# Kernel tuning notes

Measured on AMD Instinct MI355X. Metric: run time of the kernel, lower is better.

The kernel has to match this reference:

```python
import jax, jax.numpy as jnp
import numpy as np

B, S, D = 4, 2048, 768
H, K = 12, 64

def setup_inputs() -> dict:
    key = jax.random.key(0)
    k1, k2, k3, k4 = jax.random.split(key, 4)
    x = jax.random.normal(k1, (B, S, D), dtype=jnp.float32)
    Wq = jax.random.normal(k2, (H, D, K), dtype=jnp.float32) * 0.02
    Wk = jax.random.normal(k3, (H, D, K), dtype=jnp.float32) * 0.02
    Wv = jax.random.normal(k4, (H, D, K), dtype=jnp.float32) * 0.02
    return {"x": x, "Wq": Wq, "Wk": Wk, "Wv": Wv}

def reference(x, Wq, Wk, Wv):
    # per-head projections (batched over heads): [B,H,S,K]
    q = jnp.einsum('bsd,hdk->bhsk', x, Wq)
    k = jnp.einsum('bsd,hdk->bhsk', x, Wk)
    v = jnp.einsum('bsd,hdk->bhsk', x, Wv)
    scale = 1.0 / jnp.sqrt(jnp.float32(q.shape[-1]))
    scores = jnp.einsum('bhsk,bhtk->bhst', q, k) * scale  # [B,H,S,S]
    causal = jnp.tril(jnp.ones((x.shape[1], x.shape[1]), dtype=bool))
    scores = jnp.where(causal, scores, jnp.float32(-jnp.inf))
    wei = jax.nn.softmax(scores, axis=-1)
    out = jnp.einsum('bhst,bhtk->bhsk', wei, v)  # [B,H,S,K]
    # concat heads on last dim, matching torch.cat([head(x)...], dim=-1)
    b, h, s, kk = out.shape
    return out.transpose(0, 2, 1, 3).reshape(b, s, h * kk)
```

## Files before the change

### kernel.cpp

```cpp
#include <hip/hip_runtime.h>
#include <math.h>

#define BB 4
#define SS 2048
#define DD 768
#define HH 12
#define KK 64

#define NPROJ 3
#define HK    (HH * KK)
#define NCOLS (NPROJ * HK)
#define MROWS (BB * SS)
#define PER   (BB * HH * SS * KK)

typedef __attribute__((ext_vector_type(8))) short bf16x8;
typedef __attribute__((ext_vector_type(4))) short bf16x4;
typedef __attribute__((ext_vector_type(4))) float f32x4;
typedef __attribute__((ext_vector_type(16))) float f32x16;

static __device__ __forceinline__ short f2bf(float f) {
  union { float f; unsigned u; } v;
  v.f = f;
  unsigned r = (v.u + 0x7fff + ((v.u >> 16) & 1)) >> 16;
  return (short)r;
}

static __device__ __forceinline__ unsigned cvtpk(float lo, float hi) {
  unsigned r;
  asm("v_cvt_pk_bf16_f32 %0, %1, %2" : "=v"(r) : "v"(lo), "v"(hi));
  return r;
}

static __device__ __forceinline__ float fexp2(float x) {
#if __has_builtin(__builtin_amdgcn_exp2f)
  return __builtin_amdgcn_exp2f(x);
#else
  return exp2f(x);
#endif
}

__global__ __launch_bounds__(256) void conv_x(const float* __restrict__ x,
                                              short* __restrict__ xbf) {
  int i = (blockIdx.x * 256 + threadIdx.x) * 8;
  float4 v0 = *(const float4*)(x + i);
  float4 v1 = *(const float4*)(x + i + 4);
  bf16x8 o = {f2bf(v0.x), f2bf(v0.y), f2bf(v0.z), f2bf(v0.w),
              f2bf(v1.x), f2bf(v1.y), f2bf(v1.z), f2bf(v1.w)};
  *(bf16x8*)(xbf + i) = o;
}

__global__ __launch_bounds__(256) void conv_w(const float* __restrict__ Wq,
                                              const float* __restrict__ Wk,
                                              const float* __restrict__ Wv,
                                              short* __restrict__ wbf) {
  int o = blockIdx.x * 256 + threadIdx.x;
  int n = o / DD, d = o % DD;
  int proj = n / HK;
  int hk = n % HK;
  int h = hk >> 6, k = hk & 63;
  const float* W = proj == 0 ? Wq : (proj == 1 ? Wk : Wv);
  float v = W[(size_t)h * DD * KK + (size_t)d * KK + k];
  if (proj == 0) v *= 0.125f * 1.44269504088896340736f;
  wbf[o] = f2bf(v);
}

__global__ __launch_bounds__(256) void qkv_gemm(const short* __restrict__ xbf,
                                                const short* __restrict__ wbf,
                                                short* __restrict__ qkv) {
  __shared__ short smem[4 * 128 * 64];
  int bid = blockIdx.x;
  int i = bid >> 3;
  int bm = (bid & 7) * 8 + (i & 7);
  int bn = i >> 3;
  int m0 = bm * 128, n0 = bn * 128;
  int tid = threadIdx.x, lane = tid & 63, wid = tid >> 6;
  int li = lane & 15, lg = lane >> 4;
  int wm = wid >> 1, wn = wid & 1;

  f32x4 acc[4][4];
  #pragma unroll
  for (int mi = 0; mi < 4; ++mi)
    #pragma unroll
    for (int ni = 0; ni < 4; ++ni)
      acc[mi][ni] = (f32x4){0.f, 0.f, 0.f, 0.f};

  int rowoff = lane >> 3;
  int kpsw = ((lane & 7) ^ rowoff) * 8;

  #define GSTAGE(bf_, kt_)                                                     \
    {                                                                          \
      short* As_ = smem + (bf_) * 16384;                                       \
      short* Bs_ = As_ + 8192;                                                 \
      _Pragma("unroll")                                                        \
      for (int j = 0; j < 4; ++j) {                                            \
        int eb = wid * 2048 + j * 512;                                         \
        int row = (eb >> 6) + rowoff;                                          \
        __builtin_amdgcn_global_load_lds(                                      \
            (const __attribute__((address_space(1))) void*)(                   \
                xbf + (size_t)(m0 + row) * DD + (kt_) * 64 + kpsw),            \
            (__attribute__((address_space(3))) void*)(As_ + eb), 16, 0, 0);    \
        __builtin_amdgcn_global_load_lds(                                      \
            (const __attribute__((address_space(1))) void*)(                   \
                wbf + (size_t)(n0 + row) * DD + (kt_) * 64 + kpsw),            \
            (__attribute__((address_space(3))) void*)(Bs_ + eb), 16, 0, 0);    \
      }                                                                        \
    }

  GSTAGE(0, 0);

  for (int kt = 0; kt < DD / 64; ++kt) {
    int cur = kt & 1;
    if (kt + 1 < DD / 64) {
      GSTAGE(cur ^ 1, kt + 1);
      asm volatile("s_waitcnt vmcnt(8)" ::: "memory");
    } else {
      asm volatile("s_waitcnt vmcnt(0)" ::: "memory");
    }
    __builtin_amdgcn_s_barrier();

    const short* As = smem + cur * 16384;
    const short* Bs = As + 8192;
    #pragma unroll
    for (int kk = 0; kk < 2; ++kk) {
      bf16x8 af[4], bfr[4];
      #pragma unroll
      for (int mi = 0; mi < 4; ++mi)
        af[mi] = *(const bf16x8*)(As + (wm * 64 + mi * 16 + li) * 64 +
                                  (((kk * 4 + lg) ^ (li & 7)) << 3));
      #pragma unroll
      for (int ni = 0; ni < 4; ++ni)
        bfr[ni] = *(const bf16x8*)(Bs + (wn * 64 + ni * 16 + li) * 64 +
                                   (((kk * 4 + lg) ^ (li & 7)) << 3));
      #pragma unroll
      for (int mi = 0; mi < 4; ++mi)
        #pragma unroll
        for (int ni = 0; ni < 4; ++ni)
          acc[mi][ni] = __builtin_amdgcn_mfma_f32_16x16x32_bf16(
              af[mi], bfr[ni], acc[mi][ni], 0, 0, 0);
    }
    __builtin_amdgcn_s_barrier();
  }
  #undef GSTAGE

  int proj = n0 / HK;
  int hk0 = n0 % HK;
  int h0 = hk0 >> 6;

  if (proj == 2) {
    #pragma unroll
    for (int ni = 0; ni < 4; ++ni) {
      int ncol = n0 + wn * 64 + ni * 16 + li;
      int hk = ncol % HK;
      int h = hk >> 6, k = hk & 63;
      #pragma unroll
      for (int mi = 0; mi < 4; ++mi) {
        int mrow0 = m0 + wm * 64 + mi * 16 + lg * 4;
        int b = mrow0 >> 11, s = mrow0 & 2047;
        bf16x4 o = {f2bf(acc[mi][ni][0]), f2bf(acc[mi][ni][1]),
                    f2bf(acc[mi][ni][2]), f2bf(acc[mi][ni][3])};
        *(bf16x4*)(qkv + 2 * (size_t)PER +
                   ((size_t)(b * HH + h) * KK + k) * SS + s) = o;
      }
    }
  } else {
    short* Cs = smem;
    __syncthreads();
    #pragma unroll
    for (int ni = 0; ni < 4; ++ni) {
      int nl = wn * 64 + ni * 16 + li;
      int slot = nl >> 3, nlo = nl & 7;
      #pragma unroll
      for (int mi = 0; mi < 4; ++mi) {
        int ml0 = wm * 64 + mi * 16 + lg * 4;
        #pragma unroll
        for (int r = 0; r < 4; ++r) {
          int ml = ml0 + r;
          Cs[ml * 128 + ((slot ^ (ml & 7)) << 3) + nlo] =
              f2bf(acc[mi][ni][r]);
        }
      }
    }
    __syncthreads();
    int sl = tid & 7;
    #pragma unroll
    for (int p = 0; p < 8; ++p) {
      int line = p * 32 + (tid >> 3);
      int hh = line >> 7, mrow = line & 127;
      bf16x8 v = *(const bf16x8*)&Cs[mrow * 128 +
                                     (((hh * 8 + sl) ^ (mrow & 7)) << 3)];
      int gm = m0 + mrow;
      int b = gm >> 11, s = gm & 2047;
      *(bf16x8*)(qkv + (size_t)proj * PER +
                 ((size_t)(b * HH + h0 + hh) * SS + s) * KK + sl * 8) = v;
    }
  }
}

static __device__ __forceinline__ void attn_step_lds(
    const short* Kt, const short* Vv, const bf16x8* qf, bool diag, int h2,
    int lq, int hi, float& lsum, f32x16& acc0, f32x16& acc1) {
  int x7 = lq & 7;
  bf16x8 kf[4];
  {
    int kbase = (h2 * 32 + lq) * 64;
    #pragma unroll
    for (int c = 0; c < 4; ++c)
      kf[c] = *(const bf16x8*)&Kt[kbase + (((2 * c + hi) ^ x7)) * 8];
  }
  bf16x8 vf[2][2];
  #pragma unroll
  for (int m2 = 0; m2 < 2; ++m2) {
    int vbase = (32 * m2 + lq) * 64;
    #pragma unroll
    for (int c = 0; c < 2; ++c)
      vf[m2][c] =
          *(const bf16x8*)&Vv[vbase + (((h2 * 4 + 2 * c + hi) ^ x7)) * 8];
  }

  f32x16 sc;
  #pragma unroll
  for (int r = 0; r < 16; ++r) sc[r] = 0.f;
  #pragma unroll
  for (int c = 0; c < 4; ++c)
    sc = __builtin_amdgcn_mfma_f32_32x32x16_bf16(kf[c], qf[c], sc, 0, 0, 0);

  if (diag) {
    #pragma unroll
    for (int r = 0; r < 16; ++r) {
      int crow = (r & 3) + 8 * (r >> 2) + 4 * hi;
      if (crow > lq) sc[r] = -INFINITY;
    }
  }

  float p[16];
  #pragma unroll
  for (int r = 0; r < 16; ++r) p[r] = fexp2(sc[r]);

  float s8[8];
  #pragma unroll
  for (int r = 0; r < 8; ++r) s8[r] = p[2 * r] + p[2 * r + 1];
  lsum += ((s8[0] + s8[1]) + (s8[2] + s8[3])) +
          ((s8[4] + s8[5]) + (s8[6] + s8[7]));

  bf16x8 pf[2];
  #pragma unroll
  for (int c = 0; c < 2; ++c) {
    unsigned a0u = cvtpk(p[8 * c + 0], p[8 * c + 1]);
    unsigned b0u = cvtpk(p[8 * c + 4], p[8 * c + 5]);
    unsigned a1u = cvtpk(p[8 * c + 2], p[8 * c + 3]);
    unsigned b1u = cvtpk(p[8 * c + 6], p[8 * c + 7]);
    asm volatile("v_permlane32_swap_b32 %0, %1" : "+v"(a0u), "+v"(b0u));
    asm volatile("v_permlane32_swap_b32 %0, %1" : "+v"(a1u), "+v"(b1u));
    union { unsigned u[4]; bf16x8 v; } pu;
    pu.u[0] = a0u; pu.u[1] = a1u; pu.u[2] = b0u; pu.u[3] = b1u;
    pf[c] = pu.v;
  }

  acc0 = __builtin_amdgcn_mfma_f32_32x32x16_bf16(vf[0][0], pf[0], acc0, 0, 0, 0);
  acc0 = __builtin_amdgcn_mfma_f32_32x32x16_bf16(vf[0][1], pf[1], acc0, 0, 0, 0);
  acc1 = __builtin_amdgcn_mfma_f32_32x32x16_bf16(vf[1][0], pf[0], acc1, 0, 0, 0);
  acc1 = __builtin_amdgcn_mfma_f32_32x32x16_bf16(vf[1][1], pf[1], acc1, 0, 0, 0);
}

__global__ __launch_bounds__(256) void attn_kernel(
    const short* __restrict__ qkv, float* __restrict__ out) {
  __shared__ short tile[2][8192];

  int tid = threadIdx.x;
  int wid = tid >> 6, lane = tid & 63;
  int bid = blockIdx.x;
  int qb = 15 - bid / 48;
  int bh = bid % 48;
  int b = bh / HH, h = bh % HH;
  int Q0 = qb * 128;
  int s0w = Q0 + 32 * wid;
  int lq = lane & 31, hi = lane >> 5;

  const short* Qb = qkv + (size_t)bh * SS * KK;
  const short* Kb = qkv + (size_t)PER + (size_t)bh * SS * KK;
  const short* Vt = qkv + 2 * (size_t)PER + (size_t)bh * KK * SS;

  bf16x8 qf[4];
  #pragma unroll
  for (int c = 0; c < 4; ++c)
    qf[c] = *(const bf16x8*)(Qb + (size_t)(s0w + lq) * KK + c * 16 + hi * 8);

  f32x16 acc0, acc1;
  #pragma unroll
  for (int r = 0; r < 16; ++r) { acc0[r] = 0.f; acc1[r] = 0.f; }
  float lsum = 0.f;

  int srow = tid >> 3;
  int sl2 = (tid & 7) ^ (srow & 7);
  int ldsK = wid * 512;

  const int tmax = 2 * qb + 1;

  #define STAGE(bf_, t_)                                                       \
    {                                                                          \
      int kt0 = (t_) * 64;                                                     \
      _Pragma("unroll")                                                        \
      for (int i = 0; i < 2; ++i) {                                            \
        __builtin_amdgcn_global_load_lds(                                      \
            (const __attribute__((address_space(1))) void*)(                   \
                Kb + (size_t)(kt0 + i * 32 + srow) * KK + sl2 * 8),            \
            (__attribute__((address_space(3))) void*)(&tile[bf_][i * 2048 +    \
                                                                 ldsK]),       \
            16, 0, 0);                                                         \
        __builtin_amdgcn_global_load_lds(                                      \
            (const __attribute__((address_space(1))) void*)(                   \
                Vt + (size_t)(i * 32 + srow) * SS + kt0 + sl2 * 8),            \
            (__attribute__((address_space(3))) void*)(&tile[bf_][4096 +        \
                                                                 i * 2048 +    \
                                                                 ldsK]),       \
            16, 0, 0);                                                         \
      }                                                                        \
    }

  STAGE(0, 0);

  for (int t = 0; t <= tmax; ++t) {
    int cur = t & 1;
    if (t < tmax) {
      STAGE(cur ^ 1, t + 1);
      asm volatile("s_waitcnt vmcnt(4)" ::: "memory");
    } else {
      asm volatile("s_waitcnt vmcnt(0)" ::: "memory");
    }
    __builtin_amdgcn_s_barrier();

    const short* Kt = &tile[cur][0];
    const short* Vv = &tile[cur][4096];
    int kt0 = t * 64;
    #pragma unroll
    for (int h2 = 0; h2 < 2; ++h2) {
      int ks = kt0 + 32 * h2;
      if (ks <= s0w)
        attn_step_lds(Kt, Vv, qf, ks == s0w, h2, lq, hi, lsum, acc0, acc1);
    }
    __builtin_amdgcn_s_barrier();
  }
  #undef STAGE

  lsum += __shfl_xor(lsum, 32, 64);
  float inv = 1.0f / lsum;
  float* orow = out + ((size_t)(b * SS + s0w + lq)) * HK + h * KK;
  #pragma unroll
  for (int g = 0; g < 4; ++g) {
    int kd = 8 * g + 4 * hi;
    float4 w0 = {acc0[g * 4 + 0] * inv, acc0[g * 4 + 1] * inv,
                 acc0[g * 4 + 2] * inv, acc0[g * 4 + 3] * inv};
    float4 w1 = {acc1[g * 4 + 0] * inv, acc1[g * 4 + 1] * inv,
                 acc1[g * 4 + 2] * inv, acc1[g * 4 + 3] * inv};
    *(float4*)(orow + kd) = w0;
    *(float4*)(orow + 32 + kd) = w1;
  }
}

extern "C" void kernel_launch(void* const* d_in, const int* in_sizes, int n_in,
                              void* d_out, int out_size, void* d_ws,
                              size_t ws_size, hipStream_t stream) {
  const float* x  = (const float*)d_in[0];
  const float* Wq = (const float*)d_in[1];
  const float* Wk = (const float*)d_in[2];
  const float* Wv = (const float*)d_in[3];
  short* ws  = (short*)d_ws;
  short* qkv = ws;
  short* xbf = ws + (size_t)3 * PER;
  short* wbf = xbf + (size_t)MROWS * DD;
  float* o   = (float*)d_out;

  conv_x<<<(MROWS * DD) / 8 / 256, 256, 0, stream>>>(x, xbf);
  conv_w<<<(NCOLS * DD) / 256, 256, 0, stream>>>(Wq, Wk, Wv, wbf);
  qkv_gemm<<<(MROWS / 128) * (NCOLS / 128), 256, 0, stream>>>(xbf, wbf, qkv);
  attn_kernel<<<48 * 16, 256, 0, stream>>>(ws, o);
}
```

Before: 96.57 us.

## Split long causal query blocks across two KV chunks with a combine kernel

The eight longest query blocks per head are each split into two blocks, and each half processes half of the KV range. This balances work across the grid, which the causal mask otherwise skews, and raises the block count. Partial accumulators are stored as bf16 and row sums as fp32 in the now-unused xbf/wbf workspace. A new attn_norm kernel then adds the two partials and normalises them. This costs an extra launch, extra global traffic and some precision lost from bf16 partials. Combining partials without a max is valid because the kernel keeps no running max.

```diff
diff --git a/kernel.cpp b/kernel.cpp
--- a/kernel.cpp
+++ b/kernel.cpp
@@ -23,6 +23,12 @@
   v.f = f;
   unsigned r = (v.u + 0x7fff + ((v.u >> 16) & 1)) >> 16;
   return (short)r;
+}
+
+static __device__ __forceinline__ float bf2f(short s) {
+  union { unsigned u; float f; } v;
+  v.u = ((unsigned)(unsigned short)s) << 16;
+  return v.f;
 }
 
 static __device__ __forceinline__ unsigned cvtpk(float lo, float hi) {
@@ -263,17 +269,33 @@
 }
 
 __global__ __launch_bounds__(256) void attn_kernel(
-    const short* __restrict__ qkv, float* __restrict__ out) {
+    const short* __restrict__ qkv, float* __restrict__ out,
+    short* __restrict__ accP, float* __restrict__ lsumP) {
   __shared__ short tile[2][8192];
 
   int tid = threadIdx.x;
   int wid = tid >> 6, lane = tid & 63;
   int bid = blockIdx.x;
-  int qb = 15 - bid / 48;
+  int u = bid / 48;
   int bh = bid % 48;
+  int qb, tstart, tend, slot;
+  bool split;
+  if (u < 16) {
+    qb = 15 - (u >> 1);
+    int chunk = u & 1;
+    tstart = chunk * (qb + 1);
+    tend = tstart + qb;
+    slot = ((bh << 3) + (qb - 8)) * 2 + chunk;
+    split = true;
+  } else {
+    qb = 23 - u;
+    tstart = 0;
+    tend = 2 * qb + 1;
+    slot = 0;
+    split = false;
+  }
   int b = bh / HH, h = bh % HH;
-  int Q0 = qb * 128;
-  int s0w = Q0 + 32 * wid;
+  int s0w = qb * 128 + 32 * wid;
   int lq = lane & 31, hi = lane >> 5;
 
   const short* Qb = qkv + (size_t)bh * SS * KK;
@@ -293,8 +315,6 @@
   int srow = tid >> 3;
   int sl2 = (tid & 7) ^ (srow & 7);
   int ldsK = wid * 512;
-
-  const int tmax = 2 * qb + 1;
 
   #define STAGE(bf_, t_)                                                       \
     {                                                                          \
@@ -317,11 +337,11 @@
       }                                                                        \
     }
 
-  STAGE(0, 0);
-
-  for (int t = 0; t <= tmax; ++t) {
+  STAGE(tstart & 1, tstart);
+
+  for (int t = tstart; t <= tend; ++t) {
     int cur = t & 1;
-    if (t < tmax) {
+    if (t < tend) {
       STAGE(cur ^ 1, t + 1);
       asm volatile("s_waitcnt vmcnt(4)" ::: "memory");
     } else {
@@ -343,18 +363,65 @@
   #undef STAGE
 
   lsum += __shfl_xor(lsum, 32, 64);
-  float inv = 1.0f / lsum;
-  float* orow = out + ((size_t)(b * SS + s0w + lq)) * HK + h * KK;
-  #pragma unroll
-  for (int g = 0; g < 4; ++g) {
-    int kd = 8 * g + 4 * hi;
-    float4 w0 = {acc0[g * 4 + 0] * inv, acc0[g * 4 + 1] * inv,
-                 acc0[g * 4 + 2] * inv, acc0[g * 4 + 3] * inv};
-    float4 w1 = {acc1[g * 4 + 0] * inv, acc1[g * 4 + 1] * inv,
-                 acc1[g * 4 + 2] * inv, acc1[g * 4 + 3] * inv};
-    *(float4*)(orow + kd) = w0;
-    *(float4*)(orow + 32 + kd) = w1;
-  }
+
+  if (split) {
+    short* ap = accP + ((size_t)slot * 128 + 32 * wid + lq) * 64;
+    #pragma unroll
+    for (int g = 0; g < 4; ++g) {
+      int kd = 8 * g + 4 * hi;
+      union { unsigned u[2]; bf16x4 v; } p0, p1;
+      p0.u[0] = cvtpk(acc0[g * 4 + 0], acc0[g * 4 + 1]);
+      p0.u[1] = cvtpk(acc0[g * 4 + 2], acc0[g * 4 + 3]);
+      p1.u[0] = cvtpk(acc1[g * 4 + 0], acc1[g * 4 + 1]);
+      p1.u[1] = cvtpk(acc1[g * 4 + 2], acc1[g * 4 + 3]);
+      *(bf16x4*)(ap + kd) = p0.v;
+      *(bf16x4*)(ap + 32 + kd) = p1.v;
+    }
+    if (hi == 0) lsumP[slot * 128 + 32 * wid + lq] = lsum;
+  } else {
+    float inv = 1.0f / lsum;
+    float* orow = out + ((size_t)(b * SS + s0w + lq)) * HK + h * KK;
+    #pragma unroll
+    for (int g = 0; g < 4; ++g) {
+      int kd = 8 * g + 4 * hi;
+      float4 w0 = {acc0[g * 4 + 0] * inv, acc0[g * 4 + 1] * inv,
+                   acc0[g * 4 + 2] * inv, acc0[g * 4 + 3] * inv};
+      float4 w1 = {acc1[g * 4 + 0] * inv, acc1[g * 4 + 1] * inv,
+                   acc1[g * 4 + 2] * inv, acc1[g * 4 + 3] * inv};
+      *(float4*)(orow + kd) = w0;
+      *(float4*)(orow + 32 + kd) = w1;
+    }
+  }
+}
+
+__global__ __launch_bounds__(256) void attn_norm(
+    const short* __restrict__ accP, const float* __restrict__ lsumP,
+    float* __restrict__ out) {
+  int gid = blockIdx.x * 256 + threadIdx.x;
+  int kg = gid & 7;
+  int q  = (gid >> 3) & 127;
+  int t8 = gid >> 10;
+  int bh = t8 >> 3;
+  int qb = (t8 & 7) + 8;
+  int slot0 = t8 * 2;
+  const short* a0 = accP + ((size_t)slot0 * 128 + q) * 64 + kg * 8;
+  const short* a1 = a0 + (size_t)128 * 64;
+  float inv = 1.0f / (lsumP[slot0 * 128 + q] + lsumP[(slot0 + 1) * 128 + q]);
+  bf16x8 v0 = *(const bf16x8*)a0;
+  bf16x8 v1 = *(const bf16x8*)a1;
+  int b = bh / HH, h = bh % HH;
+  int s = qb * 128 + q;
+  float* orow = out + ((size_t)(b * SS + s)) * HK + h * KK + kg * 8;
+  float4 w0 = {(bf2f(v0[0]) + bf2f(v1[0])) * inv,
+               (bf2f(v0[1]) + bf2f(v1[1])) * inv,
+               (bf2f(v0[2]) + bf2f(v1[2])) * inv,
+               (bf2f(v0[3]) + bf2f(v1[3])) * inv};
+  float4 w1 = {(bf2f(v0[4]) + bf2f(v1[4])) * inv,
+               (bf2f(v0[5]) + bf2f(v1[5])) * inv,
+               (bf2f(v0[6]) + bf2f(v1[6])) * inv,
+               (bf2f(v0[7]) + bf2f(v1[7])) * inv};
+  *(float4*)(orow) = w0;
+  *(float4*)(orow + 4) = w1;
 }
 
 extern "C" void kernel_launch(void* const* d_in, const int* in_sizes, int n_in,
@@ -373,5 +440,6 @@
   conv_x<<<(MROWS * DD) / 8 / 256, 256, 0, stream>>>(x, xbf);
   conv_w<<<(NCOLS * DD) / 256, 256, 0, stream>>>(Wq, Wk, Wv, wbf);
   qkv_gemm<<<(MROWS / 128) * (NCOLS / 128), 256, 0, stream>>>(xbf, wbf, qkv);
-  attn_kernel<<<48 * 16, 256, 0, stream>>>(ws, o);
-}
+  attn_kernel<<<24 * 48, 256, 0, stream>>>(qkv, o, xbf, (float*)wbf);
+  attn_norm<<<(48 * 8 * 128 * 8) / 256, 256, 0, stream>>>(xbf, (float*)wbf, o);
+}
```

New measurement: 102.7 us. 1.06x slower.
